# Kernel tuning notes

Hardware: AMD Instinct MI355X
Metric: run time of the kernel (lower is better)

Reference implementation:

```python
import jax, jax.numpy as jnp
import numpy as np

N_PTS = 262144
N_FREQ_COOR = 10
N_FREQ_DIR = 4
D = 8
W = 256
INPUT_CH = 3 + 3 * N_FREQ_COOR * 2        # 63
INPUT_CH_DIR = 3 + 3 * N_FREQ_DIR * 2     # 27
SKIPS = (4,)
SIGMA_MUL = 0.0


def embed(x, n_freqs):
    freqs = (2.0 ** jnp.arange(n_freqs)).astype(x.dtype)      # [F]
    xf = x[..., None, :] * freqs[:, None]                      # [N, F, 3]
    sc = jnp.stack([jnp.sin(xf), jnp.cos(xf)], axis=-2)        # [N, F, 2, 3]
    sc = sc.reshape(*x.shape[:-1], n_freqs * 2 * x.shape[-1])  # [N, F*2*3]
    return jnp.concatenate([x, sc], axis=-1)


def _linear_params(key, fan_in, fan_out):
    kw, kb = jax.random.split(key)
    s = 1.0 / np.sqrt(fan_in)
    Wm = jax.random.uniform(kw, (fan_out, fan_in), jnp.float32, -s, s)
    b = jax.random.uniform(kb, (fan_out,), jnp.float32, -s, s)
    return Wm, b


def setup_inputs() -> dict:
    key = jax.random.key(0)
    keys = jax.random.split(key, 16)
    inp = {}
    inp['pts'] = jax.random.normal(keys[0], (N_PTS, 3), jnp.float32)
    inp['dirs'] = jax.random.normal(keys[1], (N_PTS, 3), jnp.float32)
    inp['dirs'] = inp['dirs'] / jnp.linalg.norm(inp['dirs'], axis=-1, keepdims=True)
    # base layer dims (skip concat before layer 5)
    dims_in = [INPUT_CH, W, W, W, W, W + INPUT_CH, W, W]
    for i in range(D):
        Wm, b = _linear_params(keys[2 + i], dims_in[i], W)
        inp[f'Wb{i}'] = Wm
        inp[f'bb{i}'] = b
    inp['Wsig'], inp['bsig'] = _linear_params(keys[10], W, 1)
    inp['Wrm'], inp['brm'] = _linear_params(keys[11], W, 256)
    inp['Wr0'], inp['br0'] = _linear_params(keys[12], 256 + INPUT_CH_DIR, W // 2)
    inp['Wr1'], inp['br1'] = _linear_params(keys[13], W // 2, 3)
    return inp


def _forward(pts, dirs,
             Wb0, bb0, Wb1, bb1, Wb2, bb2, Wb3, bb3,
             Wb4, bb4, Wb5, bb5, Wb6, bb6, Wb7, bb7,
             Wsig, bsig, Wrm, brm, Wr0, br0, Wr1, br1):
    p = embed(pts, N_FREQ_COOR)   # [N, 63]
    d = embed(dirs, N_FREQ_DIR)   # [N, 27]
    Ws = [Wb0, Wb1, Wb2, Wb3, Wb4, Wb5, Wb6, Wb7]
    bs = [bb0, bb1, bb2, bb3, bb4, bb5, bb6, bb7]
    base = jax.nn.relu(p @ Ws[0].T + bs[0])
    for i in range(D - 1):
        if i in SKIPS:
            base = jnp.concatenate([p, base], axis=-1)
        base = jax.nn.relu(base @ Ws[i + 1].T + bs[i + 1])
    sigma = base @ Wsig.T + bsig                     # [N, 1]
    sigma = sigma + jax.nn.relu(sigma) * SIGMA_MUL
    base_remap = jax.nn.relu(base @ Wrm.T + brm)     # [N, 256]
    rgb_fea = jax.nn.relu(jnp.concatenate([base_remap, d], axis=-1) @ Wr0.T + br0)
    rgb = jax.nn.sigmoid(rgb_fea @ Wr1.T + br1)      # [N, 3]
    return rgb, sigma[..., 0], d


def reference(pts, dirs,
              Wb0, bb0, Wb1, bb1, Wb2, bb2, Wb3, bb3,
              Wb4, bb4, Wb5, bb5, Wb6, bb6, Wb7, bb7,
              Wsig, bsig, Wrm, brm, Wr0, br0, Wr1, br1):
    # Returns (rgb, sigma, embedded dirs) matching StyleNerf.execute's OrderedDict values.
    return _forward(pts, dirs,
                    Wb0, bb0, Wb1, bb1, Wb2, bb2, Wb3, bb3,
                    Wb4, bb4, Wb5, bb5, Wb6, bb6, Wb7, bb7,
                    Wsig, bsig, Wrm, brm, Wr0, br0, Wr1, br1)
```

## Files before the change

### kernel.cpp

```cpp
#include <hip/hip_runtime.h>
#include <hip/hip_bf16.h>
#include <math.h>

#define NPTS 262144
#define TM   64
#define NTHR 256
#define AS   272
#define PS   80

#define WS_SHORTS 593920

typedef short  short8  __attribute__((ext_vector_type(8)));
typedef float  floatx4 __attribute__((ext_vector_type(4)));

__device__ __forceinline__ unsigned short f2b(float f) {
  union { float f; unsigned int i; } v; v.f = f;
  return (unsigned short)((v.i + 0x7fffu + ((v.i >> 16) & 1u)) >> 16);
}
__device__ __forceinline__ float b2f(unsigned short u) {
  union { unsigned int i; float f; } v; v.i = ((unsigned int)u) << 16; return v.f;
}

struct PrepArgs {
  const float* src[10];
  unsigned short* ws;
  long long dst[10];
  int steps[10];
  int ksrc[10];
  int mode[10];
  int nf16[10];
};

__global__ __launch_bounds__(256) void prep_weights(PrepArgs P) {
  int jl = blockIdx.x, c = blockIdx.y;
  if (c >= P.steps[jl]) return;
  const int NF = P.nf16[jl], tot = NF * 512;
  const float* src = P.src[jl];
  const int Ks = P.ksrc[jl], mode = P.mode[jl];
  unsigned short* dst = P.ws + P.dst[jl] + (long long)c * tot;
  for (int u = threadIdx.x; u < tot; u += 256) {
    int j = u & 7, lane = (u >> 3) & 63, nf = u >> 9;
    int n  = nf * 16 + (lane & 15);
    int kp = c * 32 + ((lane >> 4) << 3) + j;
    int sc;
    if (mode == 0)      sc = kp;
    else if (mode == 1) sc = (kp < Ks) ? kp : -1;
    else                sc = (kp < 256) ? kp + 63 : (kp < Ks ? kp - 256 : -1);
    dst[u] = (sc >= 0) ? f2b(src[(long long)n * Ks + sc]) : (unsigned short)0;
  }
}

struct NerfArgs {
  const float* pts;
  const float* dirs;
  const unsigned short* ws;
  const float* bias[10];
  const float* Wsig;
  const float* bsig;
  const float* Wr1;
  const float* br1;
  float* out;
};

template<int NFTOT, int NFW, int STEPS, int STEPS0, int LD0, int LD1>
__device__ __forceinline__ void gemm_g(
    const unsigned short* wimg,
    const short* seg0, const short* seg1,
    const float* bias, short* dst, int tid)
{
  const int lane = tid & 63, wave = tid >> 6;
  const int prow = lane & 15;
  const int r4   = (lane >> 4) * 4;
  const int koff = (lane >> 4) * 8;

  floatx4 acc[4][NFW];
  {
    float4 bv[NFW];
#pragma unroll
    for (int i = 0; i < NFW; ++i)
      bv[i] = *(const float4*)(bias + (wave * NFW + i) * 16 + r4);
#pragma unroll
    for (int mf = 0; mf < 4; ++mf)
#pragma unroll
      for (int i = 0; i < NFW; ++i) {
        acc[mf][i][0] = bv[i].x; acc[mf][i][1] = bv[i].y;
        acc[mf][i][2] = bv[i].z; acc[mf][i][3] = bv[i].w;
      }
  }

  const unsigned short* wl = wimg + (size_t)(wave * NFW) * 512 + (size_t)lane * 8;
  const short* b0 = seg0 + (size_t)prow * LD0 + koff;
  const short* b1 = seg1 + (size_t)prow * LD1 + koff;

  short8 wreg[3][NFW];
#pragma unroll
  for (int i = 0; i < NFW; ++i) wreg[0][i] = *(const short8*)(wl + i * 512);
  if (STEPS > 1) {
#pragma unroll
    for (int i = 0; i < NFW; ++i)
      wreg[1][i] = *(const short8*)(wl + (size_t)(NFTOT * 512) + i * 512);
  }

#pragma unroll
  for (int s = 0; s < STEPS; ++s) {
    if (s + 2 < STEPS) {
      const unsigned short* wn = wl + (size_t)(s + 2) * (NFTOT * 512);
#pragma unroll
      for (int i = 0; i < NFW; ++i)
        wreg[(s + 2) % 3][i] = *(const short8*)(wn + i * 512);
    }
    short8 b[4];
#pragma unroll
    for (int mf = 0; mf < 4; ++mf) {
      if (s < STEPS0) b[mf] = *(const short8*)(b0 + mf * 16 * LD0 + s * 32);
      else            b[mf] = *(const short8*)(b1 + mf * 16 * LD1 + (s - STEPS0) * 32);
    }
#pragma unroll
    for (int mf = 0; mf < 4; ++mf)
#pragma unroll
      for (int i = 0; i < NFW; ++i)
        acc[mf][i] = __builtin_amdgcn_mfma_f32_16x16x32_bf16(wreg[s % 3][i], b[mf], acc[mf][i], 0, 0, 0);
  }
  __syncthreads();
  short* dstb = dst + (size_t)prow * AS + wave * NFW * 16 + r4;
#pragma unroll
  for (int i = 0; i < NFW; ++i) {
#pragma unroll
    for (int mf = 0; mf < 4; ++mf) {
      float v0 = fmaxf(acc[mf][i][0], 0.f);
      float v1 = fmaxf(acc[mf][i][1], 0.f);
      float v2 = fmaxf(acc[mf][i][2], 0.f);
      float v3 = fmaxf(acc[mf][i][3], 0.f);
      __hip_bfloat162 h01 = __float22bfloat162_rn(make_float2(v0, v1));
      __hip_bfloat162 h23 = __float22bfloat162_rn(make_float2(v2, v3));
      int2 pk;
      pk.x = *(const int*)&h01;
      pk.y = *(const int*)&h23;
      *(int2*)(dstb + mf * 16 * AS + i * 16) = pk;
    }
  }
  __syncthreads();
}

__global__ __launch_bounds__(NTHR, 3)
void nerf_fused(NerfArgs A) {
  __shared__ alignas(16) short act[TM * AS];
  __shared__ alignas(16) short pbuf[TM * PS];
  const int tid = threadIdx.x;
  const int lane = tid & 63, wave = tid >> 6;
  const size_t gbase = (size_t)blockIdx.x * TM;

  if (tid < 192) {
    int row = tid & 63, dim = tid >> 6;
    float x = A.pts[(gbase + row) * 3 + dim];
    short* pr = pbuf + row * PS;
    pr[dim] = (short)f2b(x);
    float fr = 1.f;
    for (int q = 0; q < 10; ++q) {
      pr[3 + q * 6 + dim]     = (short)f2b(sinf(x * fr));
      pr[3 + q * 6 + 3 + dim] = (short)f2b(cosf(x * fr));
      fr *= 2.f;
    }
  } else {
    pbuf[(tid - 192) * PS + 63] = 0;
  }
  __syncthreads();

  const short* actp = act;
  short*       actw = act;
  const short* pbp  = pbuf;
  const unsigned short* ws = A.ws;

  gemm_g<16, 4,  2, 2, PS, AS>(ws + 0,      pbp,  actp, A.bias[0], actw, tid);
  gemm_g<16, 4,  8, 8, AS, AS>(ws + 16384,  actp, actp, A.bias[1], actw, tid);
  gemm_g<16, 4,  8, 8, AS, AS>(ws + 81920,  actp, actp, A.bias[2], actw, tid);
  gemm_g<16, 4,  8, 8, AS, AS>(ws + 147456, actp, actp, A.bias[3], actw, tid);
  gemm_g<16, 4,  8, 8, AS, AS>(ws + 212992, actp, actp, A.bias[4], actw, tid);
  gemm_g<16, 4, 10, 8, AS, PS>(ws + 278528, actp, pbp,  A.bias[5], actw, tid);

  if (tid >= 64 && tid < 128) {
    int row = tid - 64;
    size_t g = gbase + row;
    float x0 = A.dirs[g * 3 + 0];
    float x1 = A.dirs[g * 3 + 1];
    float x2 = A.dirs[g * 3 + 2];
    float vals[27];
    vals[0] = x0; vals[1] = x1; vals[2] = x2;
    float fr = 1.f;
    for (int q = 0; q < 4; ++q) {
      vals[3 + q * 6 + 0] = sinf(x0 * fr);
      vals[3 + q * 6 + 1] = sinf(x1 * fr);
      vals[3 + q * 6 + 2] = sinf(x2 * fr);
      vals[3 + q * 6 + 3] = cosf(x0 * fr);
      vals[3 + q * 6 + 4] = cosf(x1 * fr);
      vals[3 + q * 6 + 5] = cosf(x2 * fr);
      fr *= 2.f;
    }
    short* dr = pbuf + row * PS;
    float* og = A.out + (size_t)4 * NPTS + g * 27;
    for (int j = 0; j < 27; ++j) {
      dr[j] = (short)f2b(vals[j]);
      og[j] = vals[j];
    }
    for (int j = 27; j < 32; ++j) dr[j] = 0;
  }

  gemm_g<16, 4,  8, 8, AS, AS>(ws + 360448, actp, actp, A.bias[6], actw, tid);
  gemm_g<16, 4,  8, 8, AS, AS>(ws + 425984, actp, actp, A.bias[7], actw, tid);

  {
    int p = wave * 16 + (lane & 15);
    int q = lane >> 4;
    float s = 0.f;
    for (int c8 = 0; c8 < 8; ++c8) {
      int k0 = q * 64 + c8 * 8;
      short8 v = *(const short8*)(act + p * AS + k0);
      const float4 w0 = *(const float4*)(A.Wsig + k0);
      const float4 w1 = *(const float4*)(A.Wsig + k0 + 4);
      s += b2f((unsigned short)v[0]) * w0.x + b2f((unsigned short)v[1]) * w0.y
         + b2f((unsigned short)v[2]) * w0.z + b2f((unsigned short)v[3]) * w0.w
         + b2f((unsigned short)v[4]) * w1.x + b2f((unsigned short)v[5]) * w1.y
         + b2f((unsigned short)v[6]) * w1.z + b2f((unsigned short)v[7]) * w1.w;
    }
    s += __shfl_xor(s, 16);
    s += __shfl_xor(s, 32);
    if (q == 0) A.out[(size_t)3 * NPTS + gbase + p] = s + A.bsig[0];
  }

  gemm_g<16, 4,  8, 8, AS, AS>(ws + 491520, actp, actp, A.bias[8], actw, tid);
  gemm_g< 8, 2,  9, 8, AS, PS>(ws + 557056, actp, pbp,  A.bias[9], actw, tid);

  {
    int p = wave * 16 + (lane & 15);
    int q = lane >> 4;
    float s0 = 0.f, s1 = 0.f, s2 = 0.f;
    for (int c8 = 0; c8 < 4; ++c8) {
      int k0 = q * 32 + c8 * 8;
      short8 v = *(const short8*)(act + p * AS + k0);
#pragma unroll
      for (int j = 0; j < 8; ++j) {
        float fv = b2f((unsigned short)v[j]);
        s0 += fv * A.Wr1[k0 + j];
        s1 += fv * A.Wr1[128 + k0 + j];
        s2 += fv * A.Wr1[256 + k0 + j];
      }
    }
    s0 += __shfl_xor(s0, 16); s0 += __shfl_xor(s0, 32);
    s1 += __shfl_xor(s1, 16); s1 += __shfl_xor(s1, 32);
    s2 += __shfl_xor(s2, 16); s2 += __shfl_xor(s2, 32);
    if (q == 0) {
      size_t g = gbase + p;
      A.out[g * 3 + 0] = 1.f / (1.f + expf(-(s0 + A.br1[0])));
      A.out[g * 3 + 1] = 1.f / (1.f + expf(-(s1 + A.br1[1])));
      A.out[g * 3 + 2] = 1.f / (1.f + expf(-(s2 + A.br1[2])));
    }
  }
}

extern "C" void kernel_launch(void* const* d_in, const int* in_sizes, int n_in,
                              void* d_out, int out_size, void* d_ws, size_t ws_size,
                              hipStream_t stream) {
  PrepArgs pp;
  const int       widx[10]  = {2, 4, 6, 8, 10, 12, 14, 16, 20, 22};
  const long long doffs[10] = {0, 16384, 81920, 147456, 212992, 278528,
                               360448, 425984, 491520, 557056};
  const int stv[10] = {2, 8, 8, 8, 8, 10, 8, 8, 8, 9};
  const int ksv[10] = {63, 256, 256, 256, 256, 319, 256, 256, 256, 283};
  const int mdv[10] = {1, 0, 0, 0, 0, 2, 0, 0, 0, 1};
  const int nfv[10] = {16, 16, 16, 16, 16, 16, 16, 16, 16, 8};
  pp.ws = (unsigned short*)d_ws;
  for (int j = 0; j < 10; ++j) {
    pp.src[j] = (const float*)d_in[widx[j]];
    pp.dst[j] = doffs[j]; pp.steps[j] = stv[j]; pp.ksrc[j] = ksv[j];
    pp.mode[j] = mdv[j]; pp.nf16[j] = nfv[j];
  }
  prep_weights<<<dim3(10, 10), dim3(256), 0, stream>>>(pp);

  NerfArgs na;
  na.pts  = (const float*)d_in[0];
  na.dirs = (const float*)d_in[1];
  na.ws   = (const unsigned short*)d_ws;
  for (int i = 0; i < 8; ++i) na.bias[i] = (const float*)d_in[3 + 2 * i];
  na.bias[8] = (const float*)d_in[21];
  na.bias[9] = (const float*)d_in[23];
  na.Wsig = (const float*)d_in[18];
  na.bsig = (const float*)d_in[19];
  na.Wr1  = (const float*)d_in[24];
  na.br1  = (const float*)d_in[25];
  na.out  = (float*)d_out;
  nerf_fused<<<dim3(NPTS / TM), dim3(NTHR), 0, stream>>>(na);
}
```

Before: 404.7 us.

## Switch layer GEMMs to 32x32x16 MFMA tiles with matching weight image layout

Replaces the 16x16x32 bf16 MFMA tiling with 32x32x16 MFMA, regrouping each wave's work into 2 point tiles by NCT column tiles and re-laying out the pre-packed weight image to match. The aim is to cut LDS operand reads and instruction count per FLOP. It also changes the activation stride to 264, adds s_setprio around MFMA bursts, and replaces most sin/cos calls in positional encoding with double-angle recurrences. The recurrences can accumulate rounding error, and the new stride may add LDS bank conflicts.

```diff
diff --git a/kernel.cpp b/kernel.cpp
--- a/kernel.cpp
+++ b/kernel.cpp
@@ -5,13 +5,13 @@
 #define NPTS 262144
 #define TM   64
 #define NTHR 256
-#define AS   272
+#define AS   264
 #define PS   80
 
 #define WS_SHORTS 593920
 
 typedef short  short8  __attribute__((ext_vector_type(8)));
-typedef float  floatx4 __attribute__((ext_vector_type(4)));
+typedef float  floatx16 __attribute__((ext_vector_type(16)));
 
 __device__ __forceinline__ unsigned short f2b(float f) {
   union { float f; unsigned int i; } v; v.f = f;
@@ -28,20 +28,20 @@
   int steps[10];
   int ksrc[10];
   int mode[10];
-  int nf16[10];
+  int nf32[10];
 };
 
 __global__ __launch_bounds__(256) void prep_weights(PrepArgs P) {
   int jl = blockIdx.x, c = blockIdx.y;
   if (c >= P.steps[jl]) return;
-  const int NF = P.nf16[jl], tot = NF * 512;
+  const int NF = P.nf32[jl], tot = NF * 512;
   const float* src = P.src[jl];
   const int Ks = P.ksrc[jl], mode = P.mode[jl];
   unsigned short* dst = P.ws + P.dst[jl] + (long long)c * tot;
   for (int u = threadIdx.x; u < tot; u += 256) {
-    int j = u & 7, lane = (u >> 3) & 63, nf = u >> 9;
-    int n  = nf * 16 + (lane & 15);
-    int kp = c * 32 + ((lane >> 4) << 3) + j;
+    int j = u & 7, lane = (u >> 3) & 63, ct = u >> 9;
+    int n  = ct * 32 + (lane & 31);
+    int kp = c * 16 + ((lane >> 5) << 3) + j;
     int sc;
     if (mode == 0)      sc = kp;
     else if (mode == 1) sc = (kp < Ks) ? kp : -1;
@@ -62,42 +62,44 @@
   float* out;
 };
 
-template<int NFTOT, int NFW, int STEPS, int STEPS0, int LD0, int LD1>
-__device__ __forceinline__ void gemm_g(
+template<int NFTOT, int NCT, int STEPS, int STEPS0, int LD0, int LD1>
+__device__ __forceinline__ void gemm32(
     const unsigned short* wimg,
     const short* seg0, const short* seg1,
     const float* bias, short* dst, int tid)
 {
   const int lane = tid & 63, wave = tid >> 6;
-  const int prow = lane & 15;
-  const int r4   = (lane >> 4) * 4;
-  const int koff = (lane >> 4) * 8;
-
-  floatx4 acc[4][NFW];
-  {
-    float4 bv[NFW];
-#pragma unroll
-    for (int i = 0; i < NFW; ++i)
-      bv[i] = *(const float4*)(bias + (wave * NFW + i) * 16 + r4);
-#pragma unroll
-    for (int mf = 0; mf < 4; ++mf)
-#pragma unroll
-      for (int i = 0; i < NFW; ++i) {
-        acc[mf][i][0] = bv[i].x; acc[mf][i][1] = bv[i].y;
-        acc[mf][i][2] = bv[i].z; acc[mf][i][3] = bv[i].w;
-      }
-  }
-
-  const unsigned short* wl = wimg + (size_t)(wave * NFW) * 512 + (size_t)lane * 8;
-  const short* b0 = seg0 + (size_t)prow * LD0 + koff;
-  const short* b1 = seg1 + (size_t)prow * LD1 + koff;
-
-  short8 wreg[3][NFW];
-#pragma unroll
-  for (int i = 0; i < NFW; ++i) wreg[0][i] = *(const short8*)(wl + i * 512);
+  const int r = lane & 31;
+  const int h = lane >> 5;
+  const int koff = h * 8;
+
+  floatx16 acc[2][NCT];
+#pragma unroll
+  for (int i = 0; i < NCT; ++i) {
+    const float* bp = bias + (wave * NCT + i) * 32 + 4 * h;
+    const float4 bq0 = *(const float4*)(bp);
+    const float4 bq1 = *(const float4*)(bp + 8);
+    const float4 bq2 = *(const float4*)(bp + 16);
+    const float4 bq3 = *(const float4*)(bp + 24);
+#pragma unroll
+    for (int pt = 0; pt < 2; ++pt) {
+      acc[pt][i][0]  = bq0.x; acc[pt][i][1]  = bq0.y; acc[pt][i][2]  = bq0.z; acc[pt][i][3]  = bq0.w;
+      acc[pt][i][4]  = bq1.x; acc[pt][i][5]  = bq1.y; acc[pt][i][6]  = bq1.z; acc[pt][i][7]  = bq1.w;
+      acc[pt][i][8]  = bq2.x; acc[pt][i][9]  = bq2.y; acc[pt][i][10] = bq2.z; acc[pt][i][11] = bq2.w;
+      acc[pt][i][12] = bq3.x; acc[pt][i][13] = bq3.y; acc[pt][i][14] = bq3.z; acc[pt][i][15] = bq3.w;
+    }
+  }
+
+  const unsigned short* wl = wimg + (size_t)(wave * NCT) * 512 + (size_t)lane * 8;
+  const short* b0 = seg0 + (size_t)r * LD0 + koff;
+  const short* b1 = seg1 + (size_t)r * LD1 + koff;
+
+  short8 wreg[3][NCT];
+#pragma unroll
+  for (int i = 0; i < NCT; ++i) wreg[0][i] = *(const short8*)(wl + i * 512);
   if (STEPS > 1) {
 #pragma unroll
-    for (int i = 0; i < NFW; ++i)
+    for (int i = 0; i < NCT; ++i)
       wreg[1][i] = *(const short8*)(wl + (size_t)(NFTOT * 512) + i * 512);
   }
 
@@ -106,37 +108,42 @@
     if (s + 2 < STEPS) {
       const unsigned short* wn = wl + (size_t)(s + 2) * (NFTOT * 512);
 #pragma unroll
-      for (int i = 0; i < NFW; ++i)
+      for (int i = 0; i < NCT; ++i)
         wreg[(s + 2) % 3][i] = *(const short8*)(wn + i * 512);
     }
-    short8 b[4];
-#pragma unroll
-    for (int mf = 0; mf < 4; ++mf) {
-      if (s < STEPS0) b[mf] = *(const short8*)(b0 + mf * 16 * LD0 + s * 32);
-      else            b[mf] = *(const short8*)(b1 + mf * 16 * LD1 + (s - STEPS0) * 32);
-    }
-#pragma unroll
-    for (int mf = 0; mf < 4; ++mf)
-#pragma unroll
-      for (int i = 0; i < NFW; ++i)
-        acc[mf][i] = __builtin_amdgcn_mfma_f32_16x16x32_bf16(wreg[s % 3][i], b[mf], acc[mf][i], 0, 0, 0);
+    short8 b[2];
+#pragma unroll
+    for (int pt = 0; pt < 2; ++pt) {
+      if (s < STEPS0) b[pt] = *(const short8*)(b0 + pt * 32 * LD0 + s * 16);
+      else            b[pt] = *(const short8*)(b1 + pt * 32 * LD1 + (s - STEPS0) * 16);
+    }
+    __builtin_amdgcn_s_setprio(1);
+#pragma unroll
+    for (int pt = 0; pt < 2; ++pt)
+#pragma unroll
+      for (int i = 0; i < NCT; ++i)
+        acc[pt][i] = __builtin_amdgcn_mfma_f32_32x32x16_bf16(wreg[s % 3][i], b[pt], acc[pt][i], 0, 0, 0);
+    __builtin_amdgcn_s_setprio(0);
   }
   __syncthreads();
-  short* dstb = dst + (size_t)prow * AS + wave * NFW * 16 + r4;
-#pragma unroll
-  for (int i = 0; i < NFW; ++i) {
-#pragma unroll
-    for (int mf = 0; mf < 4; ++mf) {
-      float v0 = fmaxf(acc[mf][i][0], 0.f);
-      float v1 = fmaxf(acc[mf][i][1], 0.f);
-      float v2 = fmaxf(acc[mf][i][2], 0.f);
-      float v3 = fmaxf(acc[mf][i][3], 0.f);
-      __hip_bfloat162 h01 = __float22bfloat162_rn(make_float2(v0, v1));
-      __hip_bfloat162 h23 = __float22bfloat162_rn(make_float2(v2, v3));
-      int2 pk;
-      pk.x = *(const int*)&h01;
-      pk.y = *(const int*)&h23;
-      *(int2*)(dstb + mf * 16 * AS + i * 16) = pk;
+  short* dstb = dst + (size_t)r * AS + wave * NCT * 32 + 4 * h;
+#pragma unroll
+  for (int i = 0; i < NCT; ++i) {
+#pragma unroll
+    for (int pt = 0; pt < 2; ++pt) {
+#pragma unroll
+      for (int q = 0; q < 4; ++q) {
+        float v0 = fmaxf(acc[pt][i][4 * q + 0], 0.f);
+        float v1 = fmaxf(acc[pt][i][4 * q + 1], 0.f);
+        float v2 = fmaxf(acc[pt][i][4 * q + 2], 0.f);
+        float v3 = fmaxf(acc[pt][i][4 * q + 3], 0.f);
+        __hip_bfloat162 h01 = __float22bfloat162_rn(make_float2(v0, v1));
+        __hip_bfloat162 h23 = __float22bfloat162_rn(make_float2(v2, v3));
+        int2 pk;
+        pk.x = *(const int*)&h01;
+        pk.y = *(const int*)&h23;
+        *(int2*)(dstb + (size_t)pt * 32 * AS + i * 32 + 8 * q) = pk;
+      }
     }
   }
   __syncthreads();
@@ -155,10 +162,15 @@
     float x = A.pts[(gbase + row) * 3 + dim];
     short* pr = pbuf + row * PS;
     pr[dim] = (short)f2b(x);
-    float fr = 1.f;
+    float s = 0.f, c = 0.f, fr = 1.f;
+#pragma unroll
     for (int q = 0; q < 10; ++q) {
-      pr[3 + q * 6 + dim]     = (short)f2b(sinf(x * fr));
-      pr[3 + q * 6 + 3 + dim] = (short)f2b(cosf(x * fr));
+      if ((q & 3) == 0) { s = sinf(x * fr); c = cosf(x * fr); }
+      pr[3 + q * 6 + dim]     = (short)f2b(s);
+      pr[3 + q * 6 + 3 + dim] = (short)f2b(c);
+      float ns = 2.f * s * c;
+      float nc = 1.f - 2.f * s * s;
+      s = ns; c = nc;
       fr *= 2.f;
     }
   } else {
@@ -171,12 +183,12 @@
   const short* pbp  = pbuf;
   const unsigned short* ws = A.ws;
 
-  gemm_g<16, 4,  2, 2, PS, AS>(ws + 0,      pbp,  actp, A.bias[0], actw, tid);
-  gemm_g<16, 4,  8, 8, AS, AS>(ws + 16384,  actp, actp, A.bias[1], actw, tid);
-  gemm_g<16, 4,  8, 8, AS, AS>(ws + 81920,  actp, actp, A.bias[2], actw, tid);
-  gemm_g<16, 4,  8, 8, AS, AS>(ws + 147456, actp, actp, A.bias[3], actw, tid);
-  gemm_g<16, 4,  8, 8, AS, AS>(ws + 212992, actp, actp, A.bias[4], actw, tid);
-  gemm_g<16, 4, 10, 8, AS, PS>(ws + 278528, actp, pbp,  A.bias[5], actw, tid);
+  gemm32<8, 2,  4,  4, PS, AS>(ws + 0,      pbp,  actp, A.bias[0], actw, tid);
+  gemm32<8, 2, 16, 16, AS, AS>(ws + 16384,  actp, actp, A.bias[1], actw, tid);
+  gemm32<8, 2, 16, 16, AS, AS>(ws + 81920,  actp, actp, A.bias[2], actw, tid);
+  gemm32<8, 2, 16, 16, AS, AS>(ws + 147456, actp, actp, A.bias[3], actw, tid);
+  gemm32<8, 2, 16, 16, AS, AS>(ws + 212992, actp, actp, A.bias[4], actw, tid);
+  gemm32<8, 2, 20, 16, AS, PS>(ws + 278528, actp, pbp,  A.bias[5], actw, tid);
 
   if (tid >= 64 && tid < 128) {
     int row = tid - 64;
@@ -186,15 +198,21 @@
     float x2 = A.dirs[g * 3 + 2];
     float vals[27];
     vals[0] = x0; vals[1] = x1; vals[2] = x2;
-    float fr = 1.f;
+    float sx = sinf(x0), cx = cosf(x0);
+    float sy = sinf(x1), cy = cosf(x1);
+    float sz = sinf(x2), cz = cosf(x2);
+#pragma unroll
     for (int q = 0; q < 4; ++q) {
-      vals[3 + q * 6 + 0] = sinf(x0 * fr);
-      vals[3 + q * 6 + 1] = sinf(x1 * fr);
-      vals[3 + q * 6 + 2] = sinf(x2 * fr);
-      vals[3 + q * 6 + 3] = cosf(x0 * fr);
-      vals[3 + q * 6 + 4] = cosf(x1 * fr);
-      vals[3 + q * 6 + 5] = cosf(x2 * fr);
-      fr *= 2.f;
+      vals[3 + q * 6 + 0] = sx;
+      vals[3 + q * 6 + 1] = sy;
+      vals[3 + q * 6 + 2] = sz;
+      vals[3 + q * 6 + 3] = cx;
+      vals[3 + q * 6 + 4] = cy;
+      vals[3 + q * 6 + 5] = cz;
+      float nsx = 2.f * sx * cx, ncx = 1.f - 2.f * sx * sx;
+      float nsy = 2.f * sy * cy, ncy = 1.f - 2.f * sy * sy;
+      float nsz = 2.f * sz * cz, ncz = 1.f - 2.f * sz * sz;
+      sx = nsx; cx = ncx; sy = nsy; cy = ncy; sz = nsz; cz = ncz;
     }
     short* dr = pbuf + row * PS;
     float* og = A.out + (size_t)4 * NPTS + g * 27;
@@ -205,8 +223,8 @@
     for (int j = 27; j < 32; ++j) dr[j] = 0;
   }
 
-  gemm_g<16, 4,  8, 8, AS, AS>(ws + 360448, actp, actp, A.bias[6], actw, tid);
-  gemm_g<16, 4,  8, 8, AS, AS>(ws + 425984, actp, actp, A.bias[7], actw, tid);
+  gemm32<8, 2, 16, 16, AS, AS>(ws + 360448, actp, actp, A.bias[6], actw, tid);
+  gemm32<8, 2, 16, 16, AS, AS>(ws + 425984, actp, actp, A.bias[7], actw, tid);
 
   {
     int p = wave * 16 + (lane & 15);
@@ -227,8 +245,8 @@
     if (q == 0) A.out[(size_t)3 * NPTS + gbase + p] = s + A.bsig[0];
   }
 
-  gemm_g<16, 4,  8, 8, AS, AS>(ws + 491520, actp, actp, A.bias[8], actw, tid);
-  gemm_g< 8, 2,  9, 8, AS, PS>(ws + 557056, actp, pbp,  A.bias[9], actw, tid);
+  gemm32<8, 2, 16, 16, AS, AS>(ws + 491520, actp, actp, A.bias[8], actw, tid);
+  gemm32<4, 1, 18, 16, AS, PS>(ws + 557056, actp, pbp,  A.bias[9], actw, tid);
 
   {
     int p = wave * 16 + (lane & 15);
@@ -264,17 +282,17 @@
   const int       widx[10]  = {2, 4, 6, 8, 10, 12, 14, 16, 20, 22};
   const long long doffs[10] = {0, 16384, 81920, 147456, 212992, 278528,
                                360448, 425984, 491520, 557056};
-  const int stv[10] = {2, 8, 8, 8, 8, 10, 8, 8, 8, 9};
+  const int stv[10] = {4, 16, 16, 16, 16, 20, 16, 16, 16, 18};
   const int ksv[10] = {63, 256, 256, 256, 256, 319, 256, 256, 256, 283};
   const int mdv[10] = {1, 0, 0, 0, 0, 2, 0, 0, 0, 1};
-  const int nfv[10] = {16, 16, 16, 16, 16, 16, 16, 16, 16, 8};
+  const int nfv[10] = {8, 8, 8, 8, 8, 8, 8, 8, 8, 4};
   pp.ws = (unsigned short*)d_ws;
   for (int j = 0; j < 10; ++j) {
     pp.src[j] = (const float*)d_in[widx[j]];
     pp.dst[j] = doffs[j]; pp.steps[j] = stv[j]; pp.ksrc[j] = ksv[j];
-    pp.mode[j] = mdv[j]; pp.nf16[j] = nfv[j];
-  }
-  prep_weights<<<dim3(10, 10), dim3(256), 0, stream>>>(pp);
+    pp.mode[j] = mdv[j]; pp.nf32[j] = nfv[j];
+  }
+  prep_weights<<<dim3(10, 20), dim3(256), 0, stream>>>(pp);
 
   NerfArgs na;
   na.pts  = (const float*)d_in[0];
```

New measurement: 429.3 us. 1.06x slower.
